# Kernel optimization log

Hardware: AMD Instinct MI355X
Metric: run time of the kernel (lower is better)

The kernel has to match this reference:

```python
import jax, jax.numpy as jnp
import numpy as np

HIDDEN = 1024
NUM_HEADS = 16
HEAD_DIM = HIDDEN // NUM_HEADS


def rotate_half(x):
    x1, x2 = jnp.split(x, 2, axis=-1)
    return jnp.concatenate((-x2, x1), axis=-1)


def rope_tables(T, dim, dtype):
    inv_freq = 1.0 / (10000.0 ** (jnp.arange(0, dim, 2, dtype=jnp.float32) / dim))
    t = jnp.arange(T, dtype=jnp.float32)
    freqs = t[:, None] * inv_freq[None, :]           # [T, dim/2]
    emb = jnp.concatenate((freqs, freqs), axis=-1)   # [T, dim]
    return jnp.cos(emb).astype(dtype), jnp.sin(emb).astype(dtype)


def setup_inputs() -> dict:
    key = jax.random.key(0)
    kx, kq, kk, kv, ko = jax.random.split(key, 5)
    B, T = 2, 2048
    scale = 1.0 / np.sqrt(HIDDEN)
    return {
        "x": jax.random.normal(kx, (B, T, HIDDEN), dtype=jnp.float32),
        "wq": jax.random.normal(kq, (HIDDEN, HIDDEN), dtype=jnp.float32) * scale,
        "wk": jax.random.normal(kk, (HIDDEN, HIDDEN), dtype=jnp.float32) * scale,
        "wv": jax.random.normal(kv, (HIDDEN, HIDDEN), dtype=jnp.float32) * scale,
        "wo": jax.random.normal(ko, (HIDDEN, HIDDEN), dtype=jnp.float32) * scale,
    }


def reference(x, wq, wk, wv, wo):
    B, T, _ = x.shape
    H, D = NUM_HEADS, HEAD_DIM
    # projections (Linear, no bias): x @ W.T; reshape to [B, H, T, D]
    q = (x @ wq.T).reshape(B, T, H, D).transpose(0, 2, 1, 3)
    k = (x @ wk.T).reshape(B, T, H, D).transpose(0, 2, 1, 3)
    v = (x @ wv.T).reshape(B, T, H, D).transpose(0, 2, 1, 3)
    cos, sin = rope_tables(T, D, x.dtype)            # [T, D]
    cos = cos[None, None]                            # [1,1,T,D]
    sin = sin[None, None]
    q = q * cos + rotate_half(q) * sin
    k = k * cos + rotate_half(k) * sin
    scores = jnp.einsum("bhtd,bhsd->bhts", q, k) / np.sqrt(D).astype(x.dtype)
    attn = jax.nn.softmax(scores, axis=-1)
    out = jnp.einsum("bhts,bhsd->bhtd", attn, v)     # [B,H,T,D]
    out = out.transpose(0, 2, 1, 3).reshape(B, T, H * D)
    return out @ wo.T
```

## Files before the change

kernel.cpp:

```cpp
#include <hip/hip_runtime.h>
#include <hip/hip_bf16.h>
#include <stdint.h>

typedef __bf16 bf16;
typedef __attribute__((ext_vector_type(8))) __bf16 bf16x8;
typedef __attribute__((ext_vector_type(4))) float f32x4;
typedef __attribute__((ext_vector_type(16))) float f32x16;

#define L2E 1.4426950408889634f

__device__ __forceinline__ f32x4 mfma16(bf16x8 a, bf16x8 b, f32x4 c) {
  return __builtin_amdgcn_mfma_f32_16x16x32_bf16(a, b, c, 0, 0, 0);
}

__device__ __forceinline__ f32x16 mfma32(bf16x8 a, bf16x8 b, f32x16 c) {
  return __builtin_amdgcn_mfma_f32_32x32x16_bf16(a, b, c, 0, 0, 0);
}

__device__ __forceinline__ void gload16(void* lds, const void* g) {
  __builtin_amdgcn_global_load_lds(
      (const __attribute__((address_space(1))) uint32_t*)g,
      (__attribute__((address_space(3))) uint32_t*)lds, 16, 0, 0);
}

__device__ __forceinline__ unsigned cvt_pk_bf16(float lo, float hi) {
  unsigned r;
  asm("v_cvt_pk_bf16_f32 %0, %1, %2" : "=v"(r) : "v"(lo), "v"(hi));
  return r;
}

__device__ __forceinline__ void pl32swap(unsigned& a, unsigned& b) {
  auto r = __builtin_amdgcn_permlane32_swap(a, b, false, false);
  a = r[0];
  b = r[1];
}

__global__ __launch_bounds__(256) void prep_cast(
    const float* __restrict__ x, const float* __restrict__ wq,
    const float* __restrict__ wk, const float* __restrict__ wv,
    const float* __restrict__ wo, bf16* __restrict__ xb,
    bf16* __restrict__ wqb, bf16* __restrict__ wkb, bf16* __restrict__ wvb,
    bf16* __restrict__ wob) {
  int i = blockIdx.x * 256 + threadIdx.x;
  const int NX = 4096 * 1024 / 4;
  const int NW = 1024 * 1024 / 4;
  const float* src; bf16* dst; int off;
  if (i < NX)               { src = x;  dst = xb;  off = i; }
  else if (i < NX + NW)     { src = wq; dst = wqb; off = i - NX; }
  else if (i < NX + 2 * NW) { src = wk; dst = wkb; off = i - (NX + NW); }
  else if (i < NX + 3 * NW) { src = wv; dst = wvb; off = i - (NX + 2 * NW); }
  else                      { src = wo; dst = wob; off = i - (NX + 3 * NW); }
  float4 v = ((const float4*)src)[off];
  union { bf16 h[4]; uint2 u; } o;
  o.h[0] = (bf16)v.x; o.h[1] = (bf16)v.y; o.h[2] = (bf16)v.z; o.h[3] = (bf16)v.w;
  ((uint2*)dst)[off] = o.u;
}

__global__ __launch_bounds__(256) void rope_tab(float* __restrict__ ct,
                                                float* __restrict__ st) {
  int i = blockIdx.x * 256 + threadIdx.x;
  int t = i >> 5, d = i & 31;
  float inv = powf(10000.f, -(float)d * (1.f / 32.f));
  float a = (float)t * inv;
  ct[i] = cosf(a);
  st[i] = sinf(a);
}

__device__ __forceinline__ void gemm_mainloop(const bf16* __restrict__ A,
                                              const bf16* __restrict__ W,
                                              int m0, int n0,
                                              bf16 (*As)[4096], bf16 (*Bs)[4096],
                                              f32x4 acc[4][4]) {
  const int tid = threadIdx.x;
  const int lane = tid & 63, wave = tid >> 6;
  const int wr = (wave >> 1) * 64, wc = (wave & 1) * 64;
  const int lr = lane & 15, lh = lane >> 4;

  auto stage = [&](bf16* dA, bf16* dB, int kt) {
    int k0 = kt * 32;
#pragma unroll
    for (int p = 0; p < 2; p++) {
      int u = p * 256 + tid; int row = u >> 2; int kg = (u & 3) ^ (row & 3);
      gload16(dA + (size_t)u * 8, A + (size_t)(m0 + row) * 1024 + k0 + kg * 8);
    }
#pragma unroll
    for (int p = 0; p < 2; p++) {
      int u = p * 256 + tid; int row = u >> 2; int kg = (u & 3) ^ (row & 3);
      gload16(dB + (size_t)u * 8, W + (size_t)(n0 + row) * 1024 + k0 + kg * 8);
    }
  };

  stage(As[0], Bs[0], 0);
  int cur = 0;
  for (int kt = 0; kt < 32; ++kt) {
    __syncthreads();
    const bf16* cA = As[cur]; const bf16* cB = Bs[cur];
    bf16x8 af[4], bfr[4];
#pragma unroll
    for (int i = 0; i < 4; i++) {
      int row = wr + i * 16 + lr; int un = row * 4 + (lh ^ (row & 3));
      af[i] = *(const bf16x8*)(cA + (size_t)un * 8);
    }
#pragma unroll
    for (int j = 0; j < 4; j++) {
      int row = wc + j * 16 + lr; int un = row * 4 + (lh ^ (row & 3));
      bfr[j] = *(const bf16x8*)(cB + (size_t)un * 8);
    }
    if (kt + 1 < 32) stage(As[cur ^ 1], Bs[cur ^ 1], kt + 1);
#pragma unroll
    for (int i = 0; i < 4; i++)
#pragma unroll
      for (int j = 0; j < 4; j++) acc[i][j] = mfma16(af[i], bfr[j], acc[i][j]);
    cur ^= 1;
  }
}

__global__ __launch_bounds__(256) void gemm_qkv(
    const bf16* __restrict__ xb, const bf16* __restrict__ wq,
    const bf16* __restrict__ wk, const bf16* __restrict__ wv,
    const float* __restrict__ ct, const float* __restrict__ st,
    bf16* __restrict__ qo, bf16* __restrict__ ko, bf16* __restrict__ vo) {
  __shared__ __align__(16) bf16 As[2][4096];
  __shared__ __align__(16) bf16 Bs[2][4096];
  int bm = blockIdx.x, bn = blockIdx.y;
  int proj = bn >> 3;
  const bf16* W = proj == 0 ? wq : (proj == 1 ? wk : wv);
  bf16* out = proj == 0 ? qo : (proj == 1 ? ko : vo);
  int m0 = bm * 128, n0 = (bn & 7) * 128;

  f32x4 zero = {0.f, 0.f, 0.f, 0.f};
  f32x4 acc[4][4];
#pragma unroll
  for (int i = 0; i < 4; i++)
#pragma unroll
    for (int j = 0; j < 4; j++) acc[i][j] = zero;

  gemm_mainloop(xb, W, m0, n0, As, Bs, acc);

  const int tid = threadIdx.x, lane = tid & 63, wave = tid >> 6;
  const int wr = (wave >> 1) * 64, wc = (wave & 1) * 64;
  const int lr = lane & 15, lh = lane >> 4;
  int colb = n0 + wc;
  int h = colb >> 6;
  const float QSC = 0.125f * L2E;
#pragma unroll
  for (int i = 0; i < 4; i++) {
#pragma unroll
    for (int r = 0; r < 4; r++) {
      int m = m0 + wr + i * 16 + lh * 4 + r;
      int b = m >> 11, t = m & 2047;
      float v0 = acc[i][0][r], v1 = acc[i][1][r];
      float v2 = acc[i][2][r], v3 = acc[i][3][r];
      if (proj < 2) {
        float c0 = ct[t * 32 + lr],      s0 = st[t * 32 + lr];
        float c1 = ct[t * 32 + 16 + lr], s1 = st[t * 32 + 16 + lr];
        float n0v = v0 * c0 - v2 * s0, n2 = v2 * c0 + v0 * s0;
        float n1 = v1 * c1 - v3 * s1,  n3 = v3 * c1 + v1 * s1;
        v0 = n0v; v1 = n1; v2 = n2; v3 = n3;
        if (proj == 0) { v0 *= QSC; v1 *= QSC; v2 *= QSC; v3 *= QSC; }
      }
      size_t base = ((size_t)(b * 16 + h) * 2048 + t) * 64;
      out[base + lr]      = (bf16)v0;
      out[base + 16 + lr] = (bf16)v1;
      out[base + 32 + lr] = (bf16)v2;
      out[base + 48 + lr] = (bf16)v3;
    }
  }
}

__global__ __launch_bounds__(256) void vtrans(const bf16* __restrict__ v,
                                              bf16* __restrict__ vt) {
  __shared__ bf16 tile[64][68];
  int bh = blockIdx.x, tt = blockIdx.y;
  int tid = threadIdx.x;
  const bf16* src = v + ((size_t)bh * 2048 + tt * 64) * 64;
  int rr0 = tid >> 4;
  int c4 = (tid & 15) * 4;
#pragma unroll
  for (int p = 0; p < 4; p++) {
    int r = p * 16 + rr0;
    *(uint2*)&tile[r][c4] = *(const uint2*)(src + (size_t)r * 64 + c4);
  }
  __syncthreads();
  bf16* dst = vt + (size_t)bh * 64 * 2048 + tt * 64;
#pragma unroll
  for (int p = 0; p < 4; p++) {
    int d = p * 16 + rr0;
    union { bf16 h[4]; uint2 u; } o;
#pragma unroll
    for (int q = 0; q < 4; q++) o.h[q] = tile[c4 + q][d];
    *(uint2*)(dst + (size_t)d * 2048 + c4) = o.u;
  }
}

__global__ __launch_bounds__(256, 2) void attn(const bf16* __restrict__ q,
                                               const bf16* __restrict__ k,
                                               const bf16* __restrict__ vt,
                                               bf16* __restrict__ o) {
  __shared__ __align__(16) char smb[65536];
  int pidx = blockIdx.x;
  int L = (pidx & 7) * 64 + (pidx >> 3);
  int bh = L >> 4, qt = L & 15;

  const int tid = threadIdx.x, lane = tid & 63, wave = tid >> 6;
  const int lq = lane & 31, hi = lane >> 5;
  const int p = wave >> 1;
  const int sub = wave & 1;
  const int t128 = tid & 127;

  const bf16* kg = k + (size_t)bh * 131072 + p * 65536;
  const bf16* vg = vt + (size_t)bh * 131072 + p * 1024;

  int q0 = qt * 128 + sub * 64;
  const bf16* qbp = q + ((size_t)bh * 2048 + q0) * 64;
  bf16x8 qf[2][4];
#pragma unroll
  for (int qb = 0; qb < 2; qb++)
#pragma unroll
    for (int kk = 0; kk < 4; kk++)
      qf[qb][kk] =
          *(const bf16x8*)(qbp + (size_t)(qb * 32 + lq) * 64 + kk * 16 + hi * 8);

  int va[4];
#pragma unroll
  for (int j = 0; j < 4; j++)
    va[j] = lq * 128 + (((2 * j + hi) ^ (lq & 7)) << 4);

  int koffe[4], voffe[4];
#pragma unroll
  for (int pp = 0; pp < 4; pp++) {
    int uu = pp * 128 + t128;
    int r = uu >> 3;
    int u = (uu & 7) ^ (r & 7);
    koffe[pp] = r * 64 + u * 8;
    voffe[pp] = r * 2048 + u * 8;
  }

  f32x16 acc[2][2];
  f32x16 CM;
#pragma unroll
  for (int r = 0; r < 16; r++) {
    acc[0][0][r] = 0.f; acc[0][1][r] = 0.f;
    acc[1][0][r] = 0.f; acc[1][1][r] = 0.f;
    CM[r] = -16.f;
  }
  float l0 = 0.f, l1 = 0.f;

  const int sbase = p * 32768;
  auto stage = [&](int bufoff, int itl) {
    const bf16* kt = kg + itl * 4096;
    const bf16* vt2 = vg + itl * 64;
#pragma unroll
    for (int pp = 0; pp < 4; pp++) {
      gload16(smb + bufoff + (pp * 128 + t128) * 16, kt + koffe[pp]);
      gload16(smb + bufoff + 8192 + (pp * 128 + t128) * 16, vt2 + voffe[pp]);
    }
  };

  auto compute = [&](int bufoff) {
#pragma unroll
    for (int c = 0; c < 2; c++) {
      __builtin_amdgcn_s_setprio(1);
      bf16x8 ka[4];
#pragma unroll
      for (int kk = 0; kk < 4; kk++)
        ka[kk] = *(const bf16x8*)(smb + bufoff + c * 4096 + va[kk]);
      f32x16 s0 = mfma32(ka[0], qf[0][0], CM);
      f32x16 s1 = mfma32(ka[0], qf[1][0], CM);
#pragma unroll
      for (int kk = 1; kk < 4; kk++) {
        s0 = mfma32(ka[kk], qf[0][kk], s0);
        s1 = mfma32(ka[kk], qf[1][kk], s1);
      }
      __builtin_amdgcn_s_setprio(0);

      unsigned pk0[8], pk1[8];
      {
        float sa = 0.f, sb = 0.f;
#pragma unroll
        for (int i = 0; i < 8; i++) {
          float pa = __builtin_amdgcn_exp2f(s0[2 * i]);
          float pb = __builtin_amdgcn_exp2f(s0[2 * i + 1]);
          sa += pa; sb += pb;
          pk0[i] = cvt_pk_bf16(pa, pb);
        }
        l0 += sa + sb;
      }
      {
        float sa = 0.f, sb = 0.f;
#pragma unroll
        for (int i = 0; i < 8; i++) {
          float pa = __builtin_amdgcn_exp2f(s1[2 * i]);
          float pb = __builtin_amdgcn_exp2f(s1[2 * i + 1]);
          sa += pa; sb += pb;
          pk1[i] = cvt_pk_bf16(pa, pb);
        }
        l1 += sa + sb;
      }

      pl32swap(pk0[0], pk0[2]); pl32swap(pk0[1], pk0[3]);
      pl32swap(pk0[4], pk0[6]); pl32swap(pk0[5], pk0[7]);
      pl32swap(pk1[0], pk1[2]); pl32swap(pk1[1], pk1[3]);
      pl32swap(pk1[4], pk1[6]); pl32swap(pk1[5], pk1[7]);

      __builtin_amdgcn_s_setprio(1);
#pragma unroll
      for (int cc = 0; cc < 2; cc++) {
        union { unsigned u[4]; bf16x8 v; } pb0, pb1;
#pragma unroll
        for (int w = 0; w < 4; w++) {
          pb0.u[w] = pk0[4 * cc + w];
          pb1.u[w] = pk1[4 * cc + w];
        }
        int j = 2 * c + cc;
#pragma unroll
        for (int db = 0; db < 2; db++) {
          bf16x8 va8 =
              *(const bf16x8*)(smb + bufoff + 8192 + db * 4096 + va[j]);
          acc[0][db] = mfma32(va8, pb0.v, acc[0][db]);
          acc[1][db] = mfma32(va8, pb1.v, acc[1][db]);
        }
      }
      __builtin_amdgcn_s_setprio(0);
    }
  };

  stage(sbase, 0);
  __syncthreads();

  for (int it2 = 0; it2 < 8; ++it2) {
    stage(sbase + 16384, 2 * it2 + 1);
    compute(sbase);
    __syncthreads();
    if (it2 + 1 < 8) stage(sbase, 2 * it2 + 2);
    compute(sbase + 16384);
    __syncthreads();
  }

  float* abuf = (float*)(smb + 32768);
  float* lbuf = (float*)smb;
  if (p == 1) {
#pragma unroll
    for (int qb = 0; qb < 2; qb++)
#pragma unroll
      for (int db = 0; db < 2; db++)
#pragma unroll
        for (int r = 0; r < 16; r++)
          abuf[sub * 4096 + (qb * 2 + db) * 1024 + r * 64 + lane] =
              acc[qb][db][r];
    lbuf[sub * 128 + lane] = l0;
    lbuf[sub * 128 + 64 + lane] = l1;
  }
  __syncthreads();
  if (p == 1) return;
#pragma unroll
  for (int qb = 0; qb < 2; qb++)
#pragma unroll
    for (int db = 0; db < 2; db++)
#pragma unroll
      for (int r = 0; r < 16; r++)
        acc[qb][db][r] +=
            abuf[sub * 4096 + (qb * 2 + db) * 1024 + r * 64 + lane];
  l0 += lbuf[sub * 128 + lane];
  l1 += lbuf[sub * 128 + 64 + lane];

  {
    unsigned ta = __float_as_uint(l0), tb = __float_as_uint(l1);
    pl32swap(ta, tb);
    float inv0, inv1;
    float m0 = __uint_as_float(ta), m1 = __uint_as_float(tb);
    (void)m0; (void)m1; (void)inv0; (void)inv1;
  }
  {
    unsigned ta = __float_as_uint(l0), tb = ta;
    pl32swap(ta, tb);
    l0 = __uint_as_float(ta) + __uint_as_float(tb);
  }
  {
    unsigned ta = __float_as_uint(l1), tb = ta;
    pl32swap(ta, tb);
    l1 = __uint_as_float(ta) + __uint_as_float(tb);
  }
  float inv[2] = {1.0f / l0, 1.0f / l1};
  int b = bh >> 4, h = bh & 15;
#pragma unroll
  for (int qb = 0; qb < 2; qb++) {
    int qrow = q0 + qb * 32 + lq;
    bf16* orow = o + ((size_t)(b * 2048 + qrow)) * 1024 + h * 64;
#pragma unroll
    for (int db = 0; db < 2; db++)
#pragma unroll
      for (int g = 0; g < 4; g++) {
        union { bf16 h4[4]; uint2 u; } t;
#pragma unroll
        for (int e = 0; e < 4; e++)
          t.h4[e] = (bf16)(acc[qb][db][4 * g + e] * inv[qb]);
        *(uint2*)(orow + db * 32 + 8 * g + 4 * hi) = t.u;
      }
  }
}

__global__ __launch_bounds__(256) void gemm_out(const bf16* __restrict__ ab,
                                                const bf16* __restrict__ wo,
                                                float* __restrict__ out) {
  __shared__ __align__(16) bf16 As[2][4096];
  __shared__ __align__(16) bf16 Bs[2][4096];
  int m0 = blockIdx.x * 128, n0 = blockIdx.y * 128;
  f32x4 zero = {0.f, 0.f, 0.f, 0.f};
  f32x4 acc[4][4];
#pragma unroll
  for (int i = 0; i < 4; i++)
#pragma unroll
    for (int j = 0; j < 4; j++) acc[i][j] = zero;

  gemm_mainloop(ab, wo, m0, n0, As, Bs, acc);

  const int tid = threadIdx.x, lane = tid & 63, wave = tid >> 6;
  const int wr = (wave >> 1) * 64, wc = (wave & 1) * 64;
  const int lr = lane & 15, lh = lane >> 4;
#pragma unroll
  for (int i = 0; i < 4; i++)
#pragma unroll
    for (int r = 0; r < 4; r++) {
      int m = m0 + wr + i * 16 + lh * 4 + r;
#pragma unroll
      for (int j = 0; j < 4; j++) {
        int col = n0 + wc + j * 16 + lr;
        out[(size_t)m * 1024 + col] = acc[i][j][r];
      }
    }
}

extern "C" void kernel_launch(void* const* d_in, const int* in_sizes, int n_in,
                              void* d_out, int out_size, void* d_ws, size_t ws_size,
                              hipStream_t stream) {
  const float* x  = (const float*)d_in[0];
  const float* wq = (const float*)d_in[1];
  const float* wk = (const float*)d_in[2];
  const float* wv = (const float*)d_in[3];
  const float* wo = (const float*)d_in[4];
  float* out = (float*)d_out;
  char* ws = (char*)d_ws;
  const size_t MB = 1u << 20;
  bf16* xb  = (bf16*)(ws + 0);
  bf16* wqb = (bf16*)(ws + 8 * MB);
  bf16* wkb = (bf16*)(ws + 10 * MB);
  bf16* wvb = (bf16*)(ws + 12 * MB);
  bf16* wob = (bf16*)(ws + 14 * MB);
  bf16* qw  = (bf16*)(ws + 16 * MB);
  bf16* kw  = (bf16*)(ws + 24 * MB);
  bf16* vw  = (bf16*)(ws + 32 * MB);
  bf16* vtw = (bf16*)(ws + 40 * MB);
  bf16* aw  = (bf16*)(ws + 48 * MB);
  float* ct = (float*)(ws + 56 * MB);
  float* st = (float*)(ws + 56 * MB + 256 * 1024);

  prep_cast<<<8192, 256, 0, stream>>>(x, wq, wk, wv, wo, xb, wqb, wkb, wvb, wob);
  rope_tab<<<256, 256, 0, stream>>>(ct, st);
  gemm_qkv<<<dim3(32, 24), 256, 0, stream>>>(xb, wqb, wkb, wvb, ct, st, qw, kw, vw);
  vtrans<<<dim3(32, 32), 256, 0, stream>>>(vw, vtw);
  attn<<<512, 256, 0, stream>>>(qw, kw, vtw, aw);
  gemm_out<<<dim3(32, 8), 256, 0, stream>>>(aw, wob, out);
}
```

Measured before the change: 115.4 us.

## Fuse rope table into cast, write V transposed from QKV GEMM, restructure attention pipeline

The rope table generation moves into the prep_cast kernel as extra blocks, and the QKV GEMM epilogue writes V directly in transposed layout, so the separate rope_tab and vtrans kernels go away. This removes two launches and a full read and write of V. The attention kernel now uses a 3-stage ring buffer shared by all four waves, with waitcnt-based barriers instead of per-pair double buffering. Waves split the key tile by column chunk rather than by half of the sequence. The transposed V stores are 8-byte scattered writes, which may coalesce poorly.

Measured after the change: 116.4 us. No clear change (+0.9%).

```diff
diff --git a/kernel.cpp b/kernel.cpp
--- a/kernel.cpp
+++ b/kernel.cpp
@@ -40,8 +40,18 @@
     const float* __restrict__ wk, const float* __restrict__ wv,
     const float* __restrict__ wo, bf16* __restrict__ xb,
     bf16* __restrict__ wqb, bf16* __restrict__ wkb, bf16* __restrict__ wvb,
-    bf16* __restrict__ wob) {
-  int i = blockIdx.x * 256 + threadIdx.x;
+    bf16* __restrict__ wob, float* __restrict__ ct, float* __restrict__ st) {
+  int blk = blockIdx.x;
+  if (blk >= 8192) {
+    int i = (blk - 8192) * 256 + threadIdx.x;
+    int t = i >> 5, d = i & 31;
+    float inv = powf(10000.f, -(float)d * (1.f / 32.f));
+    float a = (float)t * inv;
+    ct[i] = cosf(a);
+    st[i] = sinf(a);
+    return;
+  }
+  int i = blk * 256 + threadIdx.x;
   const int NX = 4096 * 1024 / 4;
   const int NW = 1024 * 1024 / 4;
   const float* src; bf16* dst; int off;
@@ -56,16 +66,6 @@
   ((uint2*)dst)[off] = o.u;
 }
 
-__global__ __launch_bounds__(256) void rope_tab(float* __restrict__ ct,
-                                                float* __restrict__ st) {
-  int i = blockIdx.x * 256 + threadIdx.x;
-  int t = i >> 5, d = i & 31;
-  float inv = powf(10000.f, -(float)d * (1.f / 32.f));
-  float a = (float)t * inv;
-  ct[i] = cosf(a);
-  st[i] = sinf(a);
-}
-
 __device__ __forceinline__ void gemm_mainloop(const bf16* __restrict__ A,
                                               const bf16* __restrict__ W,
                                               int m0, int n0,
@@ -119,13 +119,12 @@
     const bf16* __restrict__ xb, const bf16* __restrict__ wq,
     const bf16* __restrict__ wk, const bf16* __restrict__ wv,
     const float* __restrict__ ct, const float* __restrict__ st,
-    bf16* __restrict__ qo, bf16* __restrict__ ko, bf16* __restrict__ vo) {
+    bf16* __restrict__ qo, bf16* __restrict__ ko, bf16* __restrict__ vto) {
   __shared__ __align__(16) bf16 As[2][4096];
   __shared__ __align__(16) bf16 Bs[2][4096];
   int bm = blockIdx.x, bn = blockIdx.y;
   int proj = bn >> 3;
   const bf16* W = proj == 0 ? wq : (proj == 1 ? wk : wv);
-  bf16* out = proj == 0 ? qo : (proj == 1 ? ko : vo);
   int m0 = bm * 128, n0 = (bn & 7) * 128;
 
   f32x4 zero = {0.f, 0.f, 0.f, 0.f};
@@ -140,6 +139,26 @@
   const int tid = threadIdx.x, lane = tid & 63, wave = tid >> 6;
   const int wr = (wave >> 1) * 64, wc = (wave & 1) * 64;
   const int lr = lane & 15, lh = lane >> 4;
+
+  if (proj == 2) {
+#pragma unroll
+    for (int i = 0; i < 4; i++) {
+      int t0 = m0 + wr + i * 16 + lh * 4;
+      int b = t0 >> 11, tt = t0 & 2047;
+#pragma unroll
+      for (int j = 0; j < 4; j++) {
+        int col = n0 + wc + j * 16 + lr;
+        int h = col >> 6, d = col & 63;
+        union { bf16 h4[4]; uint2 u; } pk4;
+#pragma unroll
+        for (int r = 0; r < 4; r++) pk4.h4[r] = (bf16)acc[i][j][r];
+        *(uint2*)(vto + ((size_t)(b * 16 + h) * 64 + d) * 2048 + tt) = pk4.u;
+      }
+    }
+    return;
+  }
+
+  bf16* out = proj == 0 ? qo : ko;
   int colb = n0 + wc;
   int h = colb >> 6;
   const float QSC = 0.125f * L2E;
@@ -151,7 +170,7 @@
       int b = m >> 11, t = m & 2047;
       float v0 = acc[i][0][r], v1 = acc[i][1][r];
       float v2 = acc[i][2][r], v3 = acc[i][3][r];
-      if (proj < 2) {
+      {
         float c0 = ct[t * 32 + lr],      s0 = st[t * 32 + lr];
         float c1 = ct[t * 32 + 16 + lr], s1 = st[t * 32 + 16 + lr];
         float n0v = v0 * c0 - v2 * s0, n2 = v2 * c0 + v0 * s0;
@@ -168,48 +187,22 @@
   }
 }
 
-__global__ __launch_bounds__(256) void vtrans(const bf16* __restrict__ v,
-                                              bf16* __restrict__ vt) {
-  __shared__ bf16 tile[64][68];
-  int bh = blockIdx.x, tt = blockIdx.y;
-  int tid = threadIdx.x;
-  const bf16* src = v + ((size_t)bh * 2048 + tt * 64) * 64;
-  int rr0 = tid >> 4;
-  int c4 = (tid & 15) * 4;
-#pragma unroll
-  for (int p = 0; p < 4; p++) {
-    int r = p * 16 + rr0;
-    *(uint2*)&tile[r][c4] = *(const uint2*)(src + (size_t)r * 64 + c4);
-  }
-  __syncthreads();
-  bf16* dst = vt + (size_t)bh * 64 * 2048 + tt * 64;
-#pragma unroll
-  for (int p = 0; p < 4; p++) {
-    int d = p * 16 + rr0;
-    union { bf16 h[4]; uint2 u; } o;
-#pragma unroll
-    for (int q = 0; q < 4; q++) o.h[q] = tile[c4 + q][d];
-    *(uint2*)(dst + (size_t)d * 2048 + c4) = o.u;
-  }
-}
-
 __global__ __launch_bounds__(256, 2) void attn(const bf16* __restrict__ q,
                                                const bf16* __restrict__ k,
                                                const bf16* __restrict__ vt,
                                                bf16* __restrict__ o) {
-  __shared__ __align__(16) char smb[65536];
+  __shared__ __align__(16) char smb[49152];
   int pidx = blockIdx.x;
   int L = (pidx & 7) * 64 + (pidx >> 3);
   int bh = L >> 4, qt = L & 15;
 
   const int tid = threadIdx.x, lane = tid & 63, wave = tid >> 6;
   const int lq = lane & 31, hi = lane >> 5;
-  const int p = wave >> 1;
   const int sub = wave & 1;
-  const int t128 = tid & 127;
-
-  const bf16* kg = k + (size_t)bh * 131072 + p * 65536;
-  const bf16* vg = vt + (size_t)bh * 131072 + p * 1024;
+  const int c = wave >> 1;
+
+  const bf16* kg = k + (size_t)bh * 131072;
+  const bf16* vg = vt + (size_t)bh * 131072;
 
   int q0 = qt * 128 + sub * 64;
   const bf16* qbp = q + ((size_t)bh * 2048 + q0) * 64;
@@ -221,19 +214,30 @@
       qf[qb][kk] =
           *(const bf16x8*)(qbp + (size_t)(qb * 32 + lq) * 64 + kk * 16 + hi * 8);
 
-  int va[4];
-#pragma unroll
-  for (int j = 0; j < 4; j++)
-    va[j] = lq * 128 + (((2 * j + hi) ^ (lq & 7)) << 4);
-
-  int koffe[4], voffe[4];
-#pragma unroll
-  for (int pp = 0; pp < 4; pp++) {
-    int uu = pp * 128 + t128;
-    int r = uu >> 3;
-    int u = (uu & 7) ^ (r & 7);
-    koffe[pp] = r * 64 + u * 8;
-    voffe[pp] = r * 2048 + u * 8;
+  int vaK[4];
+  {
+    int rowK = c * 32 + lq;
+#pragma unroll
+    for (int kk = 0; kk < 4; kk++)
+      vaK[kk] = rowK * 128 + (((2 * kk + hi) ^ (rowK & 7)) << 4);
+  }
+  int vaV[2][2];
+#pragma unroll
+  for (int cc = 0; cc < 2; cc++)
+#pragma unroll
+    for (int db = 0; db < 2; db++)
+      vaV[cc][db] = 8192 + (db * 32 + lq) * 128 +
+                    (((4 * c + 2 * cc + hi) ^ (lq & 7)) << 4);
+
+  int kofe[2], vofe[2], ldsK[2], ldsV[2];
+#pragma unroll
+  for (int pp = 0; pp < 2; pp++) {
+    int uu = pp * 256 + tid;
+    int r = uu >> 3, lu = uu & 7, su = lu ^ (r & 7);
+    kofe[pp] = r * 64 + su * 8;
+    vofe[pp] = r * 2048 + su * 8;
+    ldsK[pp] = uu * 16;
+    ldsV[pp] = 8192 + uu * 16;
   }
 
   f32x16 acc[2][2];
@@ -246,131 +250,123 @@
   }
   float l0 = 0.f, l1 = 0.f;
 
-  const int sbase = p * 32768;
-  auto stage = [&](int bufoff, int itl) {
-    const bf16* kt = kg + itl * 4096;
-    const bf16* vt2 = vg + itl * 64;
-#pragma unroll
-    for (int pp = 0; pp < 4; pp++) {
-      gload16(smb + bufoff + (pp * 128 + t128) * 16, kt + koffe[pp]);
-      gload16(smb + bufoff + 8192 + (pp * 128 + t128) * 16, vt2 + voffe[pp]);
+  auto stage = [&](int bo, int t) {
+#pragma unroll
+    for (int pp = 0; pp < 2; pp++) {
+      gload16(smb + bo + ldsK[pp], kg + t * 4096 + kofe[pp]);
+      gload16(smb + bo + ldsV[pp], vg + t * 64 + vofe[pp]);
     }
   };
 
-  auto compute = [&](int bufoff) {
-#pragma unroll
-    for (int c = 0; c < 2; c++) {
-      __builtin_amdgcn_s_setprio(1);
-      bf16x8 ka[4];
-#pragma unroll
-      for (int kk = 0; kk < 4; kk++)
-        ka[kk] = *(const bf16x8*)(smb + bufoff + c * 4096 + va[kk]);
-      f32x16 s0 = mfma32(ka[0], qf[0][0], CM);
-      f32x16 s1 = mfma32(ka[0], qf[1][0], CM);
-#pragma unroll
-      for (int kk = 1; kk < 4; kk++) {
-        s0 = mfma32(ka[kk], qf[0][kk], s0);
-        s1 = mfma32(ka[kk], qf[1][kk], s1);
-      }
-      __builtin_amdgcn_s_setprio(0);
-
-      unsigned pk0[8], pk1[8];
-      {
-        float sa = 0.f, sb = 0.f;
-#pragma unroll
-        for (int i = 0; i < 8; i++) {
-          float pa = __builtin_amdgcn_exp2f(s0[2 * i]);
-          float pb = __builtin_amdgcn_exp2f(s0[2 * i + 1]);
-          sa += pa; sb += pb;
-          pk0[i] = cvt_pk_bf16(pa, pb);
-        }
-        l0 += sa + sb;
-      }
-      {
-        float sa = 0.f, sb = 0.f;
-#pragma unroll
-        for (int i = 0; i < 8; i++) {
-          float pa = __builtin_amdgcn_exp2f(s1[2 * i]);
-          float pb = __builtin_amdgcn_exp2f(s1[2 * i + 1]);
-          sa += pa; sb += pb;
-          pk1[i] = cvt_pk_bf16(pa, pb);
-        }
-        l1 += sa + sb;
-      }
-
-      pl32swap(pk0[0], pk0[2]); pl32swap(pk0[1], pk0[3]);
-      pl32swap(pk0[4], pk0[6]); pl32swap(pk0[5], pk0[7]);
-      pl32swap(pk1[0], pk1[2]); pl32swap(pk1[1], pk1[3]);
-      pl32swap(pk1[4], pk1[6]); pl32swap(pk1[5], pk1[7]);
-
-      __builtin_amdgcn_s_setprio(1);
-#pragma unroll
-      for (int cc = 0; cc < 2; cc++) {
-        union { unsigned u[4]; bf16x8 v; } pb0, pb1;
-#pragma unroll
-        for (int w = 0; w < 4; w++) {
-          pb0.u[w] = pk0[4 * cc + w];
-          pb1.u[w] = pk1[4 * cc + w];
-        }
-        int j = 2 * c + cc;
-#pragma unroll
-        for (int db = 0; db < 2; db++) {
-          bf16x8 va8 =
-              *(const bf16x8*)(smb + bufoff + 8192 + db * 4096 + va[j]);
-          acc[0][db] = mfma32(va8, pb0.v, acc[0][db]);
-          acc[1][db] = mfma32(va8, pb1.v, acc[1][db]);
-        }
-      }
-      __builtin_amdgcn_s_setprio(0);
-    }
+  auto compute = [&](int bo) {
+    bf16x8 ka[4], vv[2][2];
+#pragma unroll
+    for (int kk = 0; kk < 4; kk++)
+      ka[kk] = *(const bf16x8*)(smb + bo + vaK[kk]);
+#pragma unroll
+    for (int cc = 0; cc < 2; cc++)
+#pragma unroll
+      for (int db = 0; db < 2; db++)
+        vv[cc][db] = *(const bf16x8*)(smb + bo + vaV[cc][db]);
+
+    __builtin_amdgcn_s_setprio(1);
+    f32x16 s0 = mfma32(ka[0], qf[0][0], CM);
+    f32x16 s1 = mfma32(ka[0], qf[1][0], CM);
+#pragma unroll
+    for (int kk = 1; kk < 4; kk++) {
+      s0 = mfma32(ka[kk], qf[0][kk], s0);
+      s1 = mfma32(ka[kk], qf[1][kk], s1);
+    }
+    __builtin_amdgcn_s_setprio(0);
+
+    unsigned pk0[8], pk1[8];
+    {
+      float sa = 0.f, sb = 0.f;
+#pragma unroll
+      for (int i = 0; i < 8; i++) {
+        float pa = __builtin_amdgcn_exp2f(s0[2 * i]);
+        float pb = __builtin_amdgcn_exp2f(s0[2 * i + 1]);
+        sa += pa; sb += pb;
+        pk0[i] = cvt_pk_bf16(pa, pb);
+      }
+      l0 += sa + sb;
+    }
+    {
+      float sa = 0.f, sb = 0.f;
+#pragma unroll
+      for (int i = 0; i < 8; i++) {
+        float pa = __builtin_amdgcn_exp2f(s1[2 * i]);
+        float pb = __builtin_amdgcn_exp2f(s1[2 * i + 1]);
+        sa += pa; sb += pb;
+        pk1[i] = cvt_pk_bf16(pa, pb);
+      }
+      l1 += sa + sb;
+    }
+
+    pl32swap(pk0[0], pk0[2]); pl32swap(pk0[1], pk0[3]);
+    pl32swap(pk0[4], pk0[6]); pl32swap(pk0[5], pk0[7]);
+    pl32swap(pk1[0], pk1[2]); pl32swap(pk1[1], pk1[3]);
+    pl32swap(pk1[4], pk1[6]); pl32swap(pk1[5], pk1[7]);
+
+    __builtin_amdgcn_s_setprio(1);
+#pragma unroll
+    for (int cc = 0; cc < 2; cc++) {
+      union { unsigned u[4]; bf16x8 v; } pb0, pb1;
+#pragma unroll
+      for (int w = 0; w < 4; w++) {
+        pb0.u[w] = pk0[4 * cc + w];
+        pb1.u[w] = pk1[4 * cc + w];
+      }
+#pragma unroll
+      for (int db = 0; db < 2; db++) {
+        acc[0][db] = mfma32(vv[cc][db], pb0.v, acc[0][db]);
+        acc[1][db] = mfma32(vv[cc][db], pb1.v, acc[1][db]);
+      }
+    }
+    __builtin_amdgcn_s_setprio(0);
   };
 
-  stage(sbase, 0);
+  stage(0, 0);
+  stage(16384, 1);
+  int boC = 0, boS = 32768;
+  for (int t = 0; t < 31; ++t) {
+    asm volatile("s_waitcnt vmcnt(4)" ::: "memory");
+    __builtin_amdgcn_s_barrier();
+    if (t + 2 < 32) stage(boS, t + 2);
+    compute(boC);
+    boC += 16384; if (boC == 49152) boC = 0;
+    boS += 16384; if (boS == 49152) boS = 0;
+  }
+  asm volatile("s_waitcnt vmcnt(0)" ::: "memory");
+  __builtin_amdgcn_s_barrier();
+  compute(boC);
+
   __syncthreads();
-
-  for (int it2 = 0; it2 < 8; ++it2) {
-    stage(sbase + 16384, 2 * it2 + 1);
-    compute(sbase);
-    __syncthreads();
-    if (it2 + 1 < 8) stage(sbase, 2 * it2 + 2);
-    compute(sbase + 16384);
-    __syncthreads();
-  }
-
-  float* abuf = (float*)(smb + 32768);
-  float* lbuf = (float*)smb;
-  if (p == 1) {
+  float* abuf = (float*)smb;
+  float* lbuf = (float*)(smb + 32768);
+  if (c == 1) {
 #pragma unroll
     for (int qb = 0; qb < 2; qb++)
 #pragma unroll
       for (int db = 0; db < 2; db++)
 #pragma unroll
         for (int r = 0; r < 16; r++)
-          abuf[sub * 4096 + (qb * 2 + db) * 1024 + r * 64 + lane] =
-              acc[qb][db][r];
-    lbuf[sub * 128 + lane] = l0;
-    lbuf[sub * 128 + 64 + lane] = l1;
+          abuf[((sub * 4 + qb * 2 + db) * 16 + r) * 64 + lane] = acc[qb][db][r];
+    lbuf[(sub * 2 + 0) * 64 + lane] = l0;
+    lbuf[(sub * 2 + 1) * 64 + lane] = l1;
   }
   __syncthreads();
-  if (p == 1) return;
+  if (c == 1) return;
 #pragma unroll
   for (int qb = 0; qb < 2; qb++)
 #pragma unroll
     for (int db = 0; db < 2; db++)
 #pragma unroll
       for (int r = 0; r < 16; r++)
-        acc[qb][db][r] +=
-            abuf[sub * 4096 + (qb * 2 + db) * 1024 + r * 64 + lane];
-  l0 += lbuf[sub * 128 + lane];
-  l1 += lbuf[sub * 128 + 64 + lane];
-
-  {
-    unsigned ta = __float_as_uint(l0), tb = __float_as_uint(l1);
-    pl32swap(ta, tb);
-    float inv0, inv1;
-    float m0 = __uint_as_float(ta), m1 = __uint_as_float(tb);
-    (void)m0; (void)m1; (void)inv0; (void)inv1;
-  }
+        acc[qb][db][r] += abuf[((sub * 4 + qb * 2 + db) * 16 + r) * 64 + lane];
+  l0 += lbuf[(sub * 2 + 0) * 64 + lane];
+  l1 += lbuf[(sub * 2 + 1) * 64 + lane];
+
   {
     unsigned ta = __float_as_uint(l0), tb = ta;
     pl32swap(ta, tb);
@@ -449,16 +445,15 @@
   bf16* wob = (bf16*)(ws + 14 * MB);
   bf16* qw  = (bf16*)(ws + 16 * MB);
   bf16* kw  = (bf16*)(ws + 24 * MB);
-  bf16* vw  = (bf16*)(ws + 32 * MB);
-  bf16* vtw = (bf16*)(ws + 40 * MB);
-  bf16* aw  = (bf16*)(ws + 48 * MB);
-  float* ct = (float*)(ws + 56 * MB);
-  float* st = (float*)(ws + 56 * MB + 256 * 1024);
-
-  prep_cast<<<8192, 256, 0, stream>>>(x, wq, wk, wv, wo, xb, wqb, wkb, wvb, wob);
-  rope_tab<<<256, 256, 0, stream>>>(ct, st);
-  gemm_qkv<<<dim3(32, 24), 256, 0, stream>>>(xb, wqb, wkb, wvb, ct, st, qw, kw, vw);
-  vtrans<<<dim3(32, 32), 256, 0, stream>>>(vw, vtw);
+  bf16* vtw = (bf16*)(ws + 32 * MB);
+  bf16* aw  = (bf16*)(ws + 40 * MB);
+  float* ct = (float*)(ws + 48 * MB);
+  float* st = (float*)(ws + 48 * MB + 256 * 1024);
+
+  prep_cast<<<8448, 256, 0, stream>>>(x, wq, wk, wv, wo, xb, wqb, wkb, wvb,
+                                      wob, ct, st);
+  gemm_qkv<<<dim3(32, 24), 256, 0, stream>>>(xb, wqb, wkb, wvb, ct, st, qw, kw,
+                                             vtw);
   attn<<<512, 256, 0, stream>>>(qw, kw, vtw, aw);
   gemm_out<<<dim3(32, 8), 256, 0, stream>>>(aw, wob, out);
 }
```
